# Performance work log

Measured on AMD Instinct MI355X. Metric: run time of the kernel, lower is better.

The kernel has to match this reference:

```python
import jax, jax.numpy as jnp
import numpy as np
from jax import lax

N, L, D, P, H, QK, VP = 1, 512, 256, 128, 8, 8, 8
FIN = H * P + H * VP * 7 + H * 7  # 1528: pair + value-point + beta features


def _l2g(R, t, p):
    # local_to_global: q = R @ p + t, applied over flattened point dims
    s = p.shape
    p3 = p.reshape(s[0], s[1], -1, 3)
    q = jnp.einsum('nlij,nlmj->nlmi', R, p3) + t[:, :, None, :]
    return q.reshape(s)


def _g2l(R, t, q):
    # global_to_local: p = R^T @ (q - t)
    s = q.shape
    q3 = q.reshape(s[0], s[1], -1, 3)
    p = jnp.einsum('nlji,nlmj->nlmi', R, q3 - t[:, :, None, :])
    return p.reshape(s)


def _inorm(x):  # InstanceNorm2d, affine=False, eps=1e-5, NCHW
    m = x.mean(axis=(2, 3), keepdims=True)
    v = x.var(axis=(2, 3), keepdims=True)
    return (x - m) * lax.rsqrt(v + 1e-5)


def _conv3(x, w, b):  # 3x3, stride 1, pad 1
    y = lax.conv_general_dilated(x, w, (1, 1), [(1, 1), (1, 1)],
                                 dimension_numbers=('NCHW', 'OIHW', 'NCHW'))
    return y + b[None, :, None, None]


def _ln(x, g, b):  # LayerNorm over last dim, eps=1e-5
    m = x.mean(-1, keepdims=True)
    v = x.var(-1, keepdims=True)
    return (x - m) * lax.rsqrt(v + 1e-5) * g + b


def _leaky(x):  # LeakyReLU, negative_slope=0.01
    return jnp.where(x >= 0, x, 0.01 * x)


def setup_inputs():
    key = jax.random.key(0)
    ks = jax.random.split(key, 24)
    s = 0.05
    return {
        'R': jax.random.normal(ks[0], (N, L, 3, 3), jnp.float32),
        't': jax.random.normal(ks[1], (N, L, 3), jnp.float32),
        'p_CB': jax.random.normal(ks[2], (N, L, 3), jnp.float32),
        'x': jax.random.normal(ks[3], (N, L, D), jnp.float32),
        'z': jax.random.normal(ks[4], (N, L, L, P), jnp.float32),
        'W_p2h': jax.random.normal(ks[5], (P, H), jnp.float32) * s,
        'gamma': jnp.ones((1, 1, H), jnp.float32),
        'Wq': jax.random.normal(ks[6], (D, H * QK * 3), jnp.float32) * s,
        'Wk': jax.random.normal(ks[7], (D, H * QK * 3), jnp.float32) * s,
        'Wv': jax.random.normal(ks[8], (D, H * VP * 3), jnp.float32) * s,
        'W1': jax.random.normal(ks[9], (FIN, 2 * D), jnp.float32) * s,
        'b1': jnp.zeros((2 * D,), jnp.float32),
        'ln1_g': jnp.ones((2 * D,), jnp.float32),
        'ln1_b': jnp.zeros((2 * D,), jnp.float32),
        'W2': jax.random.normal(ks[10], (2 * D, D), jnp.float32) * s,
        'b2': jnp.zeros((D,), jnp.float32),
        'ca_w': jax.random.normal(ks[11], (H, 2 * H, 3, 3), jnp.float32) * s,
        'ca_b': jnp.zeros((H,), jnp.float32),
        'ln_g': jnp.ones((D,), jnp.float32),
        'ln_b': jnp.zeros((D,), jnp.float32),
        'cp_w': jax.random.normal(ks[12], (P, H + P, 3, 3), jnp.float32) * s,
        'cp_b': jnp.zeros((P,), jnp.float32),
        'mask': jnp.ones((N, L), dtype=bool),
    }


def reference(R, t, p_CB, x, z, W_p2h, gamma, Wq, Wk, Wv, W1, b1, ln1_g, ln1_b,
              W2, b2, ca_w, ca_b, ln_g, ln_b, cp_w, cp_b, mask):
    n, l = x.shape[:2]
    # pair logits [n,l,l,H]
    logits_pair = jnp.einsum('nijp,ph->nijh', z, W_p2h)
    # spatial (point) logits: squared distances between global q/k points
    q_s = _l2g(R, t, (x @ Wq).reshape(n, l, H * QK, 3)).reshape(n, l, H, QK * 3)
    k_s = _l2g(R, t, (x @ Wk).reshape(n, l, H * QK, 3)).reshape(n, l, H, QK * 3)
    ssd = ((q_s ** 2).sum(-1)[:, :, None, :] + (k_s ** 2).sum(-1)[:, None, :, :]
           - 2.0 * jnp.einsum('nihd,njhd->nijh', q_s, k_s))
    logits_spatial = ssd * (-gamma * jnp.sqrt(2.0 / (9.0 * QK)) / 2.0)
    # conv2dalpha: InstanceNorm -> 3x3 conv -> LeakyReLU over the LxL grid
    lg = jnp.concatenate([logits_pair, logits_spatial], axis=-1).transpose(0, 3, 1, 2)
    logits_sum = _leaky(_conv3(_inorm(lg), ca_w, ca_b)).transpose(0, 2, 3, 1)
    mask_row = mask[:, :, None, None]
    mask_pair = mask_row & mask[:, None, :, None]
    logits_sum = jnp.where(mask_pair, logits_sum, logits_sum - 1e6)
    alpha = jax.nn.softmax(logits_sum, axis=2)
    alpha = jnp.where(mask_row, alpha, 0.0)
    # pair aggregation [n,l,H*P]
    feat_p2n = jnp.einsum('nijh,nijp->nihp', alpha, z).reshape(n, l, H * P)
    # spatial (value point) aggregation
    v_pts = _l2g(R, t, (x @ Wv).reshape(n, l, H, VP, 3))
    aggr = jnp.einsum('nijh,njhvc->nihvc', alpha, v_pts)
    fp = _g2l(R, t, aggr)  # [n,l,H,VP,3]
    fn = jnp.sqrt((fp ** 2).sum(-1))
    fdir = fp / (fn[..., None] + 1e-6)
    feat_spatial = jnp.concatenate(
        [fp.reshape(n, l, -1), fn.reshape(n, l, -1), fdir.reshape(n, l, -1)], -1)
    # beta (CB point) aggregation
    aggr_b = jnp.einsum('nijh,njc->nihc', alpha, p_CB)
    fpb = _g2l(R, t, aggr_b)  # [n,l,H,3]
    fnb = jnp.sqrt((fpb ** 2).sum(-1))
    fdb = fpb / (fnb[..., None] + 1e-6)
    feat_beta = jnp.concatenate([fpb.reshape(n, l, -1), fnb, fdb.reshape(n, l, -1)], -1)
    # out_transform: Linear -> LayerNorm -> LeakyReLU -> Linear
    feat_all = jnp.concatenate([feat_p2n, feat_spatial, feat_beta], -1)
    h1 = _leaky(_ln(feat_all @ W1 + b1, ln1_g, ln1_b))
    fa = h1 @ W2 + b2
    fa = jnp.where(mask[..., None], fa, 0.0)
    x_out = _ln(x + fa, ln_g, ln_b)
    # alpha2pair: InstanceNorm -> 3x3 conv -> LeakyReLU
    pz = jnp.concatenate([z, alpha], -1).transpose(0, 3, 1, 2)
    pair_out = _leaky(_conv3(_inorm(pz), cp_w, cp_b)).transpose(0, 2, 3, 1)
    return (x_out, pair_out)
```

## Files before the change

### kernel.cpp

```cpp
#include <hip/hip_runtime.h>
#include <hip/hip_bf16.h>
#include <math.h>

#define Lr 512
#define LL (512*512)
#define PZROW 73728

typedef __bf16 bf16x8 __attribute__((ext_vector_type(8)));
typedef float f32x16 __attribute__((ext_vector_type(16)));

static __device__ __forceinline__ unsigned short f2bf(float f) {
    union { float f; unsigned u; } a; a.f = f;
    unsigned r = a.u + 0x7fff + ((a.u >> 16) & 1);
    return (unsigned short)(r >> 16);
}

static __device__ __forceinline__ unsigned pack2(float lo, float hi) {
    return (unsigned)f2bf(lo) | ((unsigned)f2bf(hi) << 16);
}

__global__ __launch_bounds__(512) void zero_stats_k(float* lg_acc, float* pz_acc) {
    int t = threadIdx.x;
    if (t < 32) lg_acc[t] = 0.f;
    if (t < 272) pz_acc[t] = 0.f;
}

__global__ __launch_bounds__(256) void wb_prep_k(const float* __restrict__ cpw,
        const float* __restrict__ pzmr, unsigned short* __restrict__ wb) {
    int idx = blockIdx.x * 256 + threadIdx.x;
    if (idx >= 128 * 1296) return;
    int o = idx / 1296, k = idx % 1296;
    int tap = k / 144, c = k % 144;
    float v = (c < 136) ? cpw[(o * 136 + c) * 9 + tap] * pzmr[c * 2 + 1] : 0.f;
    wb[idx] = f2bf(v);
}

__global__ __launch_bounds__(128) void kc_prep_k(const float* __restrict__ cpw,
        const float* __restrict__ pzmr, float* __restrict__ kc) {
    int idx = blockIdx.x * 128 + threadIdx.x;
    if (idx >= 1152) return;
    int o = idx / 9, tap = idx % 9;
    float s = 0.f;
    for (int c = 0; c < 136; c++)
        s += cpw[(o * 136 + c) * 9 + tap] * pzmr[c * 2 + 1] * pzmr[c * 2];
    kc[idx] = -s;
}

__device__ __forceinline__ const float* qkv_colptr(const float* Wq, const float* Wk, const float* Wv, int c) {
    return c < 192 ? (Wq + c) : (c < 384 ? (Wk + c - 192) : (Wv + c - 384));
}

__global__ __launch_bounds__(256) void qkv_k(const float* __restrict__ x,
        const float* __restrict__ Wq, const float* __restrict__ Wk, const float* __restrict__ Wv,
        const float* __restrict__ R, const float* __restrict__ tv,
        float* __restrict__ qs, float* __restrict__ ks, float* __restrict__ vp,
        float* __restrict__ q2, float* __restrict__ k2) {
    __shared__ float xrow[256];
    __shared__ float praw[576];
    __shared__ float tr[576];
    __shared__ float Rt[12];
    int i = blockIdx.x, t = threadIdx.x;
    xrow[t] = x[i * 256 + t];
    if (t < 12) Rt[t] = (t < 9) ? R[i * 9 + t] : tv[i * 3 + t - 9];
    __syncthreads();
    const float* p0 = qkv_colptr(Wq, Wk, Wv, t);
    const float* p1 = qkv_colptr(Wq, Wk, Wv, t + 256);
    const float* p2 = qkv_colptr(Wq, Wk, Wv, t < 64 ? t + 512 : 575);
    float a0 = 0.f, a1 = 0.f, a2 = 0.f;
    for (int f = 0; f < 256; f++) {
        float xv = xrow[f];
        a0 += xv * p0[f * 192];
        a1 += xv * p1[f * 192];
        a2 += xv * p2[f * 192];
    }
    praw[t] = a0; praw[t + 256] = a1;
    if (t < 64) praw[t + 512] = a2;
    __syncthreads();
    if (t < 192) {
        int seg = t / 64, pt = t % 64;
        float b0 = praw[seg * 192 + pt * 3], b1_ = praw[seg * 192 + pt * 3 + 1], b2_ = praw[seg * 192 + pt * 3 + 2];
        #pragma unroll
        for (int r = 0; r < 3; r++)
            tr[seg * 192 + pt * 3 + r] = Rt[r * 3] * b0 + Rt[r * 3 + 1] * b1_ + Rt[r * 3 + 2] * b2_ + Rt[9 + r];
    }
    __syncthreads();
    if (t < 8) {
        float s = 0.f;
        #pragma unroll
        for (int d = 0; d < 24; d++) { float v = tr[t * 24 + d]; s += v * v; }
        q2[i * 8 + t] = s;
    } else if (t < 16) {
        int h = t - 8; float s = 0.f;
        #pragma unroll
        for (int d = 0; d < 24; d++) { float v = tr[192 + h * 24 + d]; s += v * v; }
        k2[i * 8 + h] = s;
    }
    for (int f = t; f < 576; f += 256) {
        float v = tr[f];
        if (f < 192) qs[i * 192 + f] = v;
        else if (f < 384) ks[i * 192 + f - 192] = v;
        else vp[i * 192 + f - 384] = v;
    }
}

__global__ __launch_bounds__(256) void zstats_pzb_k(const float4* __restrict__ z4,
        float* pz_acc, unsigned short* __restrict__ pzb) {
    __shared__ float acc[256];
    int t = threadIdx.x;
    acc[t] = 0.f;
    __syncthreads();
    int chunk = t & 15, pl = t >> 4;
    int p0 = blockIdx.x * 128;
    float s[8], s2[8];
    #pragma unroll
    for (int u = 0; u < 8; u++) { s[u] = 0.f; s2[u] = 0.f; }
    #pragma unroll
    for (int k = 0; k < 8; k++) {
        int pos = p0 + k * 16 + pl;
        const float4* src = z4 + (size_t)pos * 32 + chunk * 2;
        float4 v0 = src[0], v1 = src[1];
        float vv[8] = {v0.x, v0.y, v0.z, v0.w, v1.x, v1.y, v1.z, v1.w};
        #pragma unroll
        for (int u = 0; u < 8; u++) { s[u] += vv[u]; s2[u] += vv[u] * vv[u]; }
        uint4 q;
        q.x = pack2(vv[0], vv[1]); q.y = pack2(vv[2], vv[3]);
        q.z = pack2(vv[4], vv[5]); q.w = pack2(vv[6], vv[7]);
        int row = pos >> 9, col = pos & 511;
        *(uint4*)(pzb + ((size_t)row * 18 + chunk) * 4096 + col * 8) = q;
    }
    #pragma unroll
    for (int u = 0; u < 8; u++) {
        atomicAdd(&acc[(chunk * 8 + u) * 2], s[u]);
        atomicAdd(&acc[(chunk * 8 + u) * 2 + 1], s2[u]);
    }
    __syncthreads();
    if (t < 128) {
        atomicAdd(&pz_acc[t * 2], acc[t * 2]);
        atomicAdd(&pz_acc[t * 2 + 1], acc[t * 2 + 1]);
    }
}

__global__ __launch_bounds__(256) void lg_k(const float* __restrict__ z,
        const float* __restrict__ Wp2h, const float* __restrict__ gamma,
        const float* __restrict__ qs, const float* __restrict__ ks,
        const float* __restrict__ q2, const float* __restrict__ k2,
        float* __restrict__ lg, float* lg_acc) {
    __shared__ float zl[32 * 132];
    __shared__ float wh[8 * 132];
    __shared__ float qrow[192];
    __shared__ float q2row[8];
    __shared__ float sacc[32];
    int i = blockIdx.x, t = threadIdx.x;
    for (int f = t; f < 1024; f += 256) { int h = f >> 7, p = f & 127; wh[h * 132 + p] = Wp2h[p * 8 + h]; }
    if (t < 192) qrow[t] = qs[i * 192 + t];
    if (t < 8) q2row[t] = q2[i * 8 + t];
    if (t < 32) sacc[t] = 0.f;
    int jl = t >> 3, h = t & 7;
    float gsc = -gamma[h] * 0.08333333333333333f;
    float sp = 0.f, sp2 = 0.f, ss = 0.f, ss2 = 0.f;
    __syncthreads();
    for (int jt = 0; jt < 16; jt++) {
        int j0 = jt * 32;
        const float4* zsrc = (const float4*)(z + (size_t)(i * 512 + j0) * 128);
        #pragma unroll
        for (int r = 0; r < 4; r++) {
            int idx4 = r * 256 + t;
            int zjl = idx4 >> 5, p4 = idx4 & 31;
            *(float4*)&zl[zjl * 132 + p4 * 4] = zsrc[idx4];
        }
        __syncthreads();
        int j = j0 + jl;
        float accp = 0.f;
        const float4* za = (const float4*)&zl[jl * 132];
        const float4* wa = (const float4*)&wh[h * 132];
        #pragma unroll
        for (int p4 = 0; p4 < 32; p4++) {
            float4 a = za[p4], b = wa[p4];
            accp += a.x * b.x + a.y * b.y + a.z * b.z + a.w * b.w;
        }
        const float4* kp = (const float4*)(ks + (size_t)j * 192 + h * 24);
        const float4* qp = (const float4*)&qrow[h * 24];
        float dqk = 0.f;
        #pragma unroll
        for (int d4 = 0; d4 < 6; d4++) {
            float4 a = qp[d4], b = kp[d4];
            dqk += a.x * b.x + a.y * b.y + a.z * b.z + a.w * b.w;
        }
        float ssd = q2row[h] + k2[j * 8 + h] - 2.f * dqk;
        float lgs = ssd * gsc;
        lg[(size_t)h * LL + i * 512 + j] = accp;
        lg[(size_t)(8 + h) * LL + i * 512 + j] = lgs;
        sp += accp; sp2 += accp * accp; ss += lgs; ss2 += lgs * lgs;
        __syncthreads();
    }
    atomicAdd(&sacc[h * 2], sp);        atomicAdd(&sacc[h * 2 + 1], sp2);
    atomicAdd(&sacc[16 + h * 2], ss);   atomicAdd(&sacc[16 + h * 2 + 1], ss2);
    __syncthreads();
    if (t < 16) {
        atomicAdd(&lg_acc[t * 2], sacc[t * 2]);
        atomicAdd(&lg_acc[t * 2 + 1], sacc[t * 2 + 1]);
    }
}

__global__ void finalize_k(const float* __restrict__ acc, float* __restrict__ mr, int nch, float npix) {
    int t = threadIdx.x;
    if (t < nch) {
        float m = acc[t * 2] / npix;
        float v = acc[t * 2 + 1] / npix - m * m;
        mr[t * 2] = m;
        mr[t * 2 + 1] = rsqrtf(fmaxf(v, 0.f) + 1e-5f);
    }
}

__global__ __launch_bounds__(256) void ca_softmax_k(const float* __restrict__ lg,
        const float* __restrict__ lgmr, const float* __restrict__ caw, const float* __restrict__ cab,
        float* __restrict__ alpha, float* pz_acc, unsigned short* __restrict__ pzb) {
    __shared__ float wl[1152];
    __shared__ float mr[32];
    __shared__ float cb[8];
    __shared__ float red[64];
    int i = blockIdx.x, t = threadIdx.x;
    for (int f = t; f < 1152; f += 256) {
        int o = f & 7, k = f >> 3; int c = k / 9, r = k % 9;
        wl[f] = caw[(o * 16 + c) * 9 + r];
    }
    if (t < 32) mr[t] = lgmr[t];
    if (t < 8) cb[t] = cab[t];
    __syncthreads();
    float acc0[8], acc1[8];
    #pragma unroll
    for (int o = 0; o < 8; o++) { acc0[o] = 0.f; acc1[o] = 0.f; }
    int j0 = t, j1 = t + 256;
    const float4* w4 = (const float4*)wl;
    for (int c = 0; c < 16; c++) {
        float m = mr[c * 2], rs = mr[c * 2 + 1];
        const float* lgc = lg + (size_t)c * LL;
        #pragma unroll
        for (int di = 0; di < 3; di++) {
            int row = i - 1 + di;
            if (row < 0 || row >= 512) continue;
            const float* lr = lgc + (size_t)row * 512;
            float v0[3], v1[3];
            v0[0] = (j0 > 0) ? (lr[j0 - 1] - m) * rs : 0.f;
            v0[1] = (lr[j0] - m) * rs;
            v0[2] = (lr[j0 + 1] - m) * rs;
            v1[0] = (lr[j1 - 1] - m) * rs;
            v1[1] = (lr[j1] - m) * rs;
            v1[2] = (j1 < 511) ? (lr[j1 + 1] - m) * rs : 0.f;
            int wb = (c * 9 + di * 3) * 2;
            #pragma unroll
            for (int dj = 0; dj < 3; dj++) {
                float4 wa = w4[wb + dj * 2], wbv = w4[wb + dj * 2 + 1];
                acc0[0] += wa.x * v0[dj]; acc0[1] += wa.y * v0[dj]; acc0[2] += wa.z * v0[dj]; acc0[3] += wa.w * v0[dj];
                acc0[4] += wbv.x * v0[dj]; acc0[5] += wbv.y * v0[dj]; acc0[6] += wbv.z * v0[dj]; acc0[7] += wbv.w * v0[dj];
                acc1[0] += wa.x * v1[dj]; acc1[1] += wa.y * v1[dj]; acc1[2] += wa.z * v1[dj]; acc1[3] += wa.w * v1[dj];
                acc1[4] += wbv.x * v1[dj]; acc1[5] += wbv.y * v1[dj]; acc1[6] += wbv.z * v1[dj]; acc1[7] += wbv.w * v1[dj];
            }
        }
    }
    float s0[8], s1[8];
    #pragma unroll
    for (int o = 0; o < 8; o++) {
        float v = acc0[o] + cb[o]; s0[o] = v >= 0.f ? v : 0.01f * v;
        float w = acc1[o] + cb[o]; s1[o] = w >= 0.f ? w : 0.01f * w;
    }
    int lane = t & 63, wid = t >> 6;
    float mx[8];
    #pragma unroll
    for (int o = 0; o < 8; o++) mx[o] = fmaxf(s0[o], s1[o]);
    for (int off = 1; off < 64; off <<= 1) {
        #pragma unroll
        for (int o = 0; o < 8; o++) mx[o] = fmaxf(mx[o], __shfl_xor(mx[o], off));
    }
    if (lane == 0) {
        #pragma unroll
        for (int o = 0; o < 8; o++) red[wid * 8 + o] = mx[o];
    }
    __syncthreads();
    float M[8];
    #pragma unroll
    for (int o = 0; o < 8; o++) M[o] = fmaxf(fmaxf(red[o], red[8 + o]), fmaxf(red[16 + o], red[24 + o]));
    float e0[8], e1[8], sm[8];
    #pragma unroll
    for (int o = 0; o < 8; o++) { e0[o] = expf(s0[o] - M[o]); e1[o] = expf(s1[o] - M[o]); sm[o] = e0[o] + e1[o]; }
    __syncthreads();
    for (int off = 1; off < 64; off <<= 1) {
        #pragma unroll
        for (int o = 0; o < 8; o++) sm[o] += __shfl_xor(sm[o], off);
    }
    if (lane == 0) {
        #pragma unroll
        for (int o = 0; o < 8; o++) red[wid * 8 + o] = sm[o];
    }
    __syncthreads();
    float a0[8], a1[8], st_s[8], st_q[8];
    #pragma unroll
    for (int o = 0; o < 8; o++) {
        float rden = 1.f / (red[o] + red[8 + o] + red[16 + o] + red[24 + o]);
        a0[o] = e0[o] * rden; a1[o] = e1[o] * rden;
        st_s[o] = a0[o] + a1[o];
        st_q[o] = a0[o] * a0[o] + a1[o] * a1[o];
    }
    size_t base = (size_t)i * 512;
    #pragma unroll
    for (int o = 0; o < 8; o++) {
        alpha[(size_t)o * LL + base + t] = a0[o];
        alpha[(size_t)o * LL + base + t + 256] = a1[o];
    }
    {
        uint4 p0, p1;
        p0.x = pack2(a0[0], a0[1]); p0.y = pack2(a0[2], a0[3]);
        p0.z = pack2(a0[4], a0[5]); p0.w = pack2(a0[6], a0[7]);
        p1.x = pack2(a1[0], a1[1]); p1.y = pack2(a1[2], a1[3]);
        p1.z = pack2(a1[4], a1[5]); p1.w = pack2(a1[6], a1[7]);
        unsigned short* pb = pzb + (size_t)i * PZROW + 16 * 4096;
        *(uint4*)(pb + (size_t)t * 8) = p0;
        *(uint4*)(pb + (size_t)(t + 256) * 8) = p1;
        uint4 zz = {0u, 0u, 0u, 0u};
        *(uint4*)(pb + 4096 + (size_t)t * 8) = zz;
        *(uint4*)(pb + 4096 + (size_t)(t + 256) * 8) = zz;
    }
    __syncthreads();
    for (int off = 1; off < 64; off <<= 1) {
        #pragma unroll
        for (int o = 0; o < 8; o++) { st_s[o] += __shfl_xor(st_s[o], off); st_q[o] += __shfl_xor(st_q[o], off); }
    }
    if (lane == 0) {
        #pragma unroll
        for (int o = 0; o < 8; o++) { red[wid * 8 + o] = st_s[o]; red[32 + wid * 8 + o] = st_q[o]; }
    }
    __syncthreads();
    if (t < 8) {
        float ts = red[t] + red[8 + t] + red[16 + t] + red[24 + t];
        float tq = red[32 + t] + red[40 + t] + red[48 + t] + red[56 + t];
        atomicAdd(&pz_acc[(128 + t) * 2], ts);
        atomicAdd(&pz_acc[(128 + t) * 2 + 1], tq);
    }
}

__global__ __launch_bounds__(256) void feat_mlp_k(
        const float* __restrict__ alpha, const float* __restrict__ z,
        const float* __restrict__ vp, const float* __restrict__ pcb,
        const float* __restrict__ R, const float* __restrict__ tv,
        const float* __restrict__ W1, const float* __restrict__ b1,
        const float* __restrict__ ln1g, const float* __restrict__ ln1b,
        const float* __restrict__ W2, const float* __restrict__ b2,
        const float* __restrict__ lng, const float* __restrict__ lnb,
        const float* __restrict__ x, float* __restrict__ xout) {
    __shared__ float al[8 * 512];
    __shared__ float zl[64 * 128];
    __shared__ float feat[1536];
    __shared__ float h1[512];
    __shared__ float agg[216];
    __shared__ float Rt[12];
    __shared__ float redl[8];
    int i = blockIdx.x, t = threadIdx.x;
    for (int f = t; f < 4096; f += 256) al[f] = alpha[(size_t)(f >> 9) * LL + i * 512 + (f & 511)];
    if (t < 12) Rt[t] = (t < 9) ? R[i * 9 + t] : tv[i * 3 + t - 9];
    __syncthreads();
    if (t < 216) {
        float a = 0.f;
        if (t < 192) {
            int h = t / 24;
            const float* vptr = vp + t;
            const float* ar = al + h * 512;
            for (int j = 0; j < 512; j++) a += ar[j] * vptr[(size_t)j * 192];
        } else {
            int u = t - 192; int h = u / 3, cc = u % 3;
            const float* ar = al + h * 512;
            for (int j = 0; j < 512; j++) a += ar[j] * pcb[j * 3 + cc];
        }
        agg[t] = a;
    }
    float4 accp = {0.f, 0.f, 0.f, 0.f};
    int hh = t >> 5, p4 = t & 31;
    for (int jc = 0; jc < 8; jc++) {
        const float4* zsrc = (const float4*)(z + (size_t)(i * 512 + jc * 64) * 128);
        #pragma unroll
        for (int r = 0; r < 8; r++) ((float4*)zl)[r * 256 + t] = zsrc[r * 256 + t];
        __syncthreads();
        const float* ar = al + hh * 512 + jc * 64;
        const float4* zv = (const float4*)zl + p4;
        #pragma unroll 4
        for (int jl = 0; jl < 64; jl++) {
            float a = ar[jl];
            float4 v = zv[jl * 32];
            accp.x += a * v.x; accp.y += a * v.y; accp.z += a * v.z; accp.w += a * v.w;
        }
        __syncthreads();
    }
    *(float4*)&feat[hh * 128 + p4 * 4] = accp;
    __syncthreads();
    if (t < 64) {
        int h = t >> 3, v = t & 7;
        float d0 = agg[h * 24 + v * 3] - Rt[9];
        float d1 = agg[h * 24 + v * 3 + 1] - Rt[10];
        float d2 = agg[h * 24 + v * 3 + 2] - Rt[11];
        float f0 = Rt[0] * d0 + Rt[3] * d1 + Rt[6] * d2;
        float f1 = Rt[1] * d0 + Rt[4] * d1 + Rt[7] * d2;
        float f2 = Rt[2] * d0 + Rt[5] * d1 + Rt[8] * d2;
        float n = sqrtf(f0 * f0 + f1 * f1 + f2 * f2);
        float rn = 1.f / (n + 1e-6f);
        feat[1024 + h * 24 + v * 3] = f0;
        feat[1024 + h * 24 + v * 3 + 1] = f1;
        feat[1024 + h * 24 + v * 3 + 2] = f2;
        feat[1216 + h * 8 + v] = n;
        feat[1280 + h * 24 + v * 3] = f0 * rn;
        feat[1280 + h * 24 + v * 3 + 1] = f1 * rn;
        feat[1280 + h * 24 + v * 3 + 2] = f2 * rn;
    } else if (t < 72) {
        int h = t - 64;
        float d0 = agg[192 + h * 3] - Rt[9];
        float d1 = agg[192 + h * 3 + 1] - Rt[10];
        float d2 = agg[192 + h * 3 + 2] - Rt[11];
        float f0 = Rt[0] * d0 + Rt[3] * d1 + Rt[6] * d2;
        float f1 = Rt[1] * d0 + Rt[4] * d1 + Rt[7] * d2;
        float f2 = Rt[2] * d0 + Rt[5] * d1 + Rt[8] * d2;
        float n = sqrtf(f0 * f0 + f1 * f1 + f2 * f2);
        float rn = 1.f / (n + 1e-6f);
        feat[1472 + h * 3] = f0; feat[1472 + h * 3 + 1] = f1; feat[1472 + h * 3 + 2] = f2;
        feat[1496 + h] = n;
        feat[1504 + h * 3] = f0 * rn; feat[1504 + h * 3 + 1] = f1 * rn; feat[1504 + h * 3 + 2] = f2 * rn;
    }
    __syncthreads();
    float acc0 = b1[t], acc1 = b1[t + 256];
    const float4* f4 = (const float4*)feat;
    for (int f = 0; f < 1528; f += 4) {
        float4 fv = f4[f >> 2];
        const float* w = W1 + (size_t)f * 512 + t;
        acc0 += fv.x * w[0] + fv.y * w[512] + fv.z * w[1024] + fv.w * w[1536];
        const float* w2p = w + 256;
        acc1 += fv.x * w2p[0] + fv.y * w2p[512] + fv.z * w2p[1024] + fv.w * w2p[1536];
    }
    int lane = t & 63, wid = t >> 6;
    float s = acc0 + acc1, s2 = acc0 * acc0 + acc1 * acc1;
    for (int off = 1; off < 64; off <<= 1) { s += __shfl_xor(s, off); s2 += __shfl_xor(s2, off); }
    if (lane == 0) { redl[wid * 2] = s; redl[wid * 2 + 1] = s2; }
    __syncthreads();
    float S = redl[0] + redl[2] + redl[4] + redl[6];
    float S2 = redl[1] + redl[3] + redl[5] + redl[7];
    float mean = S / 512.f;
    float rstd = rsqrtf(fmaxf(S2 / 512.f - mean * mean, 0.f) + 1e-5f);
    float hv0 = (acc0 - mean) * rstd * ln1g[t] + ln1b[t];
    float hv1 = (acc1 - mean) * rstd * ln1g[t + 256] + ln1b[t + 256];
    hv0 = hv0 >= 0.f ? hv0 : 0.01f * hv0;
    hv1 = hv1 >= 0.f ? hv1 : 0.01f * hv1;
    h1[t] = hv0; h1[t + 256] = hv1;
    __syncthreads();
    float a2 = b2[t];
    const float4* h14 = (const float4*)h1;
    for (int k = 0; k < 512; k += 4) {
        float4 hv = h14[k >> 2];
        const float* w = W2 + (size_t)k * 256 + t;
        a2 += hv.x * w[0] + hv.y * w[256] + hv.z * w[512] + hv.w * w[768];
    }
    float xv = x[i * 256 + t] + a2;
    float ss_ = xv, sq_ = xv * xv;
    for (int off = 1; off < 64; off <<= 1) { ss_ += __shfl_xor(ss_, off); sq_ += __shfl_xor(sq_, off); }
    __syncthreads();
    if (lane == 0) { redl[wid * 2] = ss_; redl[wid * 2 + 1] = sq_; }
    __syncthreads();
    float Sx = redl[0] + redl[2] + redl[4] + redl[6];
    float Sx2 = redl[1] + redl[3] + redl[5] + redl[7];
    float mx = Sx / 256.f;
    float rsx = rsqrtf(fmaxf(Sx2 / 256.f - mx * mx, 0.f) + 1e-5f);
    xout[i * 256 + t] = (xv - mx) * rsx * lng[t] + lnb[t];
}

__global__ __launch_bounds__(256) void conv_mfma_k(
        const unsigned short* __restrict__ pzb, const unsigned short* __restrict__ wb,
        const float* __restrict__ kc, const float* __restrict__ cpb,
        float* __restrict__ pout) {
    __shared__ unsigned short abuf[2368 * 8];
    __shared__ float csA[128];
    __shared__ float cs0[128];
    __shared__ float cs2[128];
    int t = threadIdx.x;
    int bid = blockIdx.x;
    int swz = (bid & 7) * 256 + (bid >> 3);
    int i = swz >> 2;
    int j0 = (swz & 3) * 128;
    if (t < 128) {
        int o = t;
        float a0 = 0.f, a1 = 0.f, a2 = 0.f;
        #pragma unroll
        for (int di = 0; di < 3; di++) {
            int grow = i - 1 + di;
            if (grow < 0 || grow > 511) continue;
            a0 += kc[o * 9 + di * 3];
            a1 += kc[o * 9 + di * 3 + 1];
            a2 += kc[o * 9 + di * 3 + 2];
        }
        cs0[o] = a0; cs2[o] = a2; csA[o] = cpb[o] + a0 + a1 + a2;
    }
    int w = t >> 6, lane = t & 63;
    int l31 = lane & 31, lhi = lane >> 5;
    int mt0 = (w & 1) * 64;
    int nt0 = (w >> 1) * 64;

    uint4 rg[10];
    #define STAGE_LOAD(DI) do {                                                \
        int grow_ = i - 1 + (DI);                                              \
        bool rowok_ = (grow_ >= 0 && grow_ < 512);                             \
        const unsigned short* rowp_ = pzb + (size_t)grow_ * PZROW;             \
        _Pragma("unroll")                                                      \
        for (int k = 0; k < 10; k++) {                                         \
            int f_ = t + k * 256;                                              \
            uint4 v_ = {0u, 0u, 0u, 0u};                                       \
            if (f_ < 2340) {                                                   \
                int c_ = f_ / 130, col_ = f_ - c_ * 130;                       \
                int gcol_ = j0 - 1 + col_;                                     \
                if (rowok_ && (unsigned)gcol_ < 512u)                          \
                    v_ = *(const uint4*)(rowp_ + c_ * 4096 + gcol_ * 8);       \
            }                                                                  \
            rg[k] = v_;                                                        \
        }                                                                      \
    } while (0)

    #define STAGE_WRITE() do {                                                 \
        _Pragma("unroll")                                                      \
        for (int k = 0; k < 10; k++) {                                         \
            int f_ = t + k * 256;                                              \
            if (f_ < 2340) *(uint4*)(abuf + f_ * 8) = rg[k];                   \
        }                                                                      \
    } while (0)

    f32x16 acc00 = {}, acc01 = {}, acc10 = {}, acc11 = {};

    STAGE_LOAD(0);
    STAGE_WRITE();
    __syncthreads();

    #pragma unroll
    for (int di = 0; di < 3; di++) {
        if (di < 2) STAGE_LOAD(di + 1);
        #pragma unroll
        for (int dj = 0; dj < 3; dj++) {
            int tap = di * 3 + dj;
            const unsigned short* wp0 = wb + (size_t)(nt0 + l31) * 1296 + tap * 144 + lhi * 8;
            const unsigned short* wp1 = wp0 + 32 * 1296;
            const unsigned short* ap0 = abuf + lhi * 1040 + (mt0 + l31 + dj) * 8;
            const unsigned short* ap1 = ap0 + 256;
            #pragma unroll
            for (int ksn = 0; ksn < 9; ksn++) {
                bf16x8 a0 = *(const bf16x8*)(ap0 + ksn * 2080);
                bf16x8 a1 = *(const bf16x8*)(ap1 + ksn * 2080);
                bf16x8 b0 = *(const bf16x8*)(wp0 + ksn * 16);
                bf16x8 b1 = *(const bf16x8*)(wp1 + ksn * 16);
                acc00 = __builtin_amdgcn_mfma_f32_32x32x16_bf16(a0, b0, acc00, 0, 0, 0);
                acc01 = __builtin_amdgcn_mfma_f32_32x32x16_bf16(a0, b1, acc01, 0, 0, 0);
                acc10 = __builtin_amdgcn_mfma_f32_32x32x16_bf16(a1, b0, acc10, 0, 0, 0);
                acc11 = __builtin_amdgcn_mfma_f32_32x32x16_bf16(a1, b1, acc11, 0, 0, 0);
            }
        }
        __syncthreads();
        if (di < 2) {
            STAGE_WRITE();
            __syncthreads();
        }
    }
    #undef STAGE_LOAD
    #undef STAGE_WRITE

    #pragma unroll
    for (int mi = 0; mi < 2; mi++) {
        #pragma unroll
        for (int ni = 0; ni < 2; ni++) {
            const f32x16* a = (mi == 0) ? (ni == 0 ? &acc00 : &acc01) : (ni == 0 ? &acc10 : &acc11);
            int nb = nt0 + ni * 32 + l31;
            float bA = csA[nb], b0_ = cs0[nb], b2_ = cs2[nb];
            #pragma unroll
            for (int r = 0; r < 16; r++) {
                int m = mt0 + mi * 32 + 4 * lhi + (r & 3) + 8 * (r >> 2);
                int j = j0 + m;
                float bias = bA - (j == 0 ? b0_ : 0.f) - (j == 511 ? b2_ : 0.f);
                float v = (*a)[r] + bias;
                v = v >= 0.f ? v : 0.01f * v;
                pout[((size_t)(i * 512 + j)) * 128 + nb] = v;
            }
        }
    }
}

extern "C" void kernel_launch(void* const* d_in, const int* in_sizes, int n_in,
                              void* d_out, int out_size, void* d_ws, size_t ws_size,
                              hipStream_t stream) {
    (void)in_sizes; (void)n_in; (void)out_size; (void)ws_size;
    const float* R    = (const float*)d_in[0];
    const float* tv   = (const float*)d_in[1];
    const float* pcb  = (const float*)d_in[2];
    const float* x    = (const float*)d_in[3];
    const float* z    = (const float*)d_in[4];
    const float* wp2h = (const float*)d_in[5];
    const float* gamma= (const float*)d_in[6];
    const float* Wq   = (const float*)d_in[7];
    const float* Wk   = (const float*)d_in[8];
    const float* Wv   = (const float*)d_in[9];
    const float* W1   = (const float*)d_in[10];
    const float* b1   = (const float*)d_in[11];
    const float* ln1g = (const float*)d_in[12];
    const float* ln1b = (const float*)d_in[13];
    const float* W2   = (const float*)d_in[14];
    const float* b2   = (const float*)d_in[15];
    const float* caw  = (const float*)d_in[16];
    const float* cab  = (const float*)d_in[17];
    const float* lng  = (const float*)d_in[18];
    const float* lnb  = (const float*)d_in[19];
    const float* cpw  = (const float*)d_in[20];
    const float* cpb  = (const float*)d_in[21];

    float* ws = (float*)d_ws;
    float* qs     = ws;
    float* ksv    = qs + 98304;
    float* vp     = ksv + 98304;
    float* q2     = vp + 98304;
    float* k2     = q2 + 4096;
    float* lg_acc = k2 + 4096;
    float* lg_mr  = lg_acc + 32;
    float* pz_acc = lg_mr + 32;
    float* pz_mr  = pz_acc + 272;
    float* kc     = pz_mr + 272;
    unsigned short* wbq = (unsigned short*)(kc + 1152);
    float* lg     = kc + 1152 + 82944;
    float* alpha  = lg + 16 * LL;
    unsigned short* pzb = (unsigned short*)(alpha + 8 * LL);

    float* xout = (float*)d_out;
    float* pout = xout + 131072;

    hipLaunchKernelGGL(zero_stats_k, dim3(1), dim3(512), 0, stream, lg_acc, pz_acc);
    hipLaunchKernelGGL(qkv_k, dim3(512), dim3(256), 0, stream, x, Wq, Wk, Wv, R, tv, qs, ksv, vp, q2, k2);
    hipLaunchKernelGGL(zstats_pzb_k, dim3(2048), dim3(256), 0, stream, (const float4*)z, pz_acc, pzb);
    hipLaunchKernelGGL(lg_k, dim3(512), dim3(256), 0, stream, z, wp2h, gamma, qs, ksv, q2, k2, lg, lg_acc);
    hipLaunchKernelGGL(finalize_k, dim3(1), dim3(64), 0, stream, lg_acc, lg_mr, 16, 262144.f);
    hipLaunchKernelGGL(ca_softmax_k, dim3(512), dim3(256), 0, stream, lg, lg_mr, caw, cab, alpha, pz_acc, pzb);
    hipLaunchKernelGGL(finalize_k, dim3(1), dim3(192), 0, stream, pz_acc, pz_mr, 136, 262144.f);
    hipLaunchKernelGGL(wb_prep_k, dim3(648), dim3(256), 0, stream, cpw, pz_mr, wbq);
    hipLaunchKernelGGL(kc_prep_k, dim3(9), dim3(128), 0, stream, cpw, pz_mr, kc);
    hipLaunchKernelGGL(feat_mlp_k, dim3(512), dim3(256), 0, stream,
                       alpha, z, vp, pcb, R, tv, W1, b1, ln1g, ln1b, W2, b2, lng, lnb, x, xout);
    hipLaunchKernelGGL(conv_mfma_k, dim3(2048), dim3(256), 0, stream, pzb, wbq, kc, cpb, pout);
}
```

Baseline: 775.0 us.

## Reorder conv weight layout for coalesced B loads and stage output through LDS

Rewrites the bf16 conv weight buffer into a tap/k-slice/lane-interleaved layout so each wave's B-fragment loads read contiguous memory instead of strided rows. It also changes the epilogue: accumulators are written to an LDS tile per 64-row half and then copied out with coalesced float4 stores, replacing scattered per-element global writes. This adds two extra barriers per half and reuses the A staging buffer as scratch.

```diff
diff --git a/kernel.cpp b/kernel.cpp
--- a/kernel.cpp
+++ b/kernel.cpp
@@ -29,9 +29,14 @@
         const float* __restrict__ pzmr, unsigned short* __restrict__ wb) {
     int idx = blockIdx.x * 256 + threadIdx.x;
     if (idx >= 128 * 1296) return;
-    int o = idx / 1296, k = idx % 1296;
-    int tap = k / 144, c = k % 144;
-    float v = (c < 136) ? cpw[(o * 136 + c) * 9 + tap] * pzmr[c * 2 + 1] : 0.f;
+    int j = idx & 7;
+    int n = (idx >> 3) & 127;
+    int rest = idx >> 10;
+    int lhi = rest & 1;
+    int ksn = (rest >> 1) % 9;
+    int tap = rest / 18;
+    int c = ksn * 16 + lhi * 8 + j;
+    float v = (c < 136) ? cpw[(n * 136 + c) * 9 + tap] * pzmr[c * 2 + 1] : 0.f;
     wb[idx] = f2bf(v);
 }
 
@@ -537,16 +542,15 @@
         #pragma unroll
         for (int dj = 0; dj < 3; dj++) {
             int tap = di * 3 + dj;
-            const unsigned short* wp0 = wb + (size_t)(nt0 + l31) * 1296 + tap * 144 + lhi * 8;
-            const unsigned short* wp1 = wp0 + 32 * 1296;
+            const unsigned short* wt = wb + (size_t)(tap * 18 + lhi) * 1024 + (nt0 + l31) * 8;
             const unsigned short* ap0 = abuf + lhi * 1040 + (mt0 + l31 + dj) * 8;
             const unsigned short* ap1 = ap0 + 256;
             #pragma unroll
             for (int ksn = 0; ksn < 9; ksn++) {
                 bf16x8 a0 = *(const bf16x8*)(ap0 + ksn * 2080);
                 bf16x8 a1 = *(const bf16x8*)(ap1 + ksn * 2080);
-                bf16x8 b0 = *(const bf16x8*)(wp0 + ksn * 16);
-                bf16x8 b1 = *(const bf16x8*)(wp1 + ksn * 16);
+                bf16x8 b0 = *(const bf16x8*)(wt + ksn * 2048);
+                bf16x8 b1 = *(const bf16x8*)(wt + ksn * 2048 + 256);
                 acc00 = __builtin_amdgcn_mfma_f32_32x32x16_bf16(a0, b0, acc00, 0, 0, 0);
                 acc01 = __builtin_amdgcn_mfma_f32_32x32x16_bf16(a0, b1, acc01, 0, 0, 0);
                 acc10 = __builtin_amdgcn_mfma_f32_32x32x16_bf16(a1, b0, acc10, 0, 0, 0);
@@ -562,23 +566,38 @@
     #undef STAGE_LOAD
     #undef STAGE_WRITE
 
-    #pragma unroll
-    for (int mi = 0; mi < 2; mi++) {
-        #pragma unroll
-        for (int ni = 0; ni < 2; ni++) {
-            const f32x16* a = (mi == 0) ? (ni == 0 ? &acc00 : &acc01) : (ni == 0 ? &acc10 : &acc11);
-            int nb = nt0 + ni * 32 + l31;
-            float bA = csA[nb], b0_ = cs0[nb], b2_ = cs2[nb];
+    float* fb = (float*)abuf;
+    #pragma unroll
+    for (int mh = 0; mh < 2; mh++) {
+        if ((w & 1) == mh) {
             #pragma unroll
-            for (int r = 0; r < 16; r++) {
-                int m = mt0 + mi * 32 + 4 * lhi + (r & 3) + 8 * (r >> 2);
-                int j = j0 + m;
-                float bias = bA - (j == 0 ? b0_ : 0.f) - (j == 511 ? b2_ : 0.f);
-                float v = (*a)[r] + bias;
-                v = v >= 0.f ? v : 0.01f * v;
-                pout[((size_t)(i * 512 + j)) * 128 + nb] = v;
+            for (int mi = 0; mi < 2; mi++) {
+                #pragma unroll
+                for (int ni = 0; ni < 2; ni++) {
+                    const f32x16* a = (mi == 0) ? (ni == 0 ? &acc00 : &acc01) : (ni == 0 ? &acc10 : &acc11);
+                    int nb = nt0 + ni * 32 + l31;
+                    float bA = csA[nb], b0_ = cs0[nb], b2_ = cs2[nb];
+                    #pragma unroll
+                    for (int r = 0; r < 16; r++) {
+                        int ml = mi * 32 + 4 * lhi + (r & 3) + 8 * (r >> 2);
+                        int j = j0 + mh * 64 + ml;
+                        float bias = bA - (j == 0 ? b0_ : 0.f) - (j == 511 ? b2_ : 0.f);
+                        float v = (*a)[r] + bias;
+                        v = v >= 0.f ? v : 0.01f * v;
+                        fb[ml * 128 + nb] = v;
+                    }
+                }
             }
         }
+        __syncthreads();
+        const float4* fb4 = (const float4*)fb;
+        float4* gdst = (float4*)(pout + ((size_t)(i * 512 + j0 + mh * 64)) * 128);
+        #pragma unroll
+        for (int k = 0; k < 8; k++) {
+            int f4i = k * 256 + t;
+            gdst[f4i] = fb4[f4i];
+        }
+        __syncthreads();
     }
 }
 
```

Result: no change. 773.7 us (-0.2%).
